# Optimization experiments

Measured on AMD Instinct MI355X. Metric: run time of the kernel, lower is better.

The kernel has to match this reference:

```python
import jax, jax.numpy as jnp
import numpy as np
import math

B, L, D_IN, D, H, NL, FF = 8, 1024, 32, 512, 8, 6, 64
DK = D // H

def _ln(x, g, b, eps=1e-5):
    m = jnp.mean(x, axis=-1, keepdims=True)
    v = jnp.mean((x - m) ** 2, axis=-1, keepdims=True)
    return (x - m) * jax.lax.rsqrt(v + eps) * g + b

def setup_inputs() -> dict:
    key = jax.random.key(0)
    ks = jax.random.split(key, 32)
    def nrm(k, shape, s=0.02):
        return jax.random.normal(k, shape, jnp.float32) * s
    x = jax.random.normal(ks[0], (B, L, D_IN), jnp.float32)
    mask = jnp.broadcast_to(jnp.tril(jnp.ones((L, L), jnp.int32))[None], (B, L, L))
    obs_time = jnp.arange(B * L, dtype=jnp.float32).reshape(B, L)
    inp = {
        "x": x, "mask": mask, "obs_time": obs_time,
        # embedding MLP: Linear(d_input,d) -> ReLU -> [Dropout] -> LayerNorm -> Linear(d,d)
        "emb_w1": nrm(ks[1], (D_IN, D)), "emb_b1": jnp.zeros((D,), jnp.float32),
        "emb_g": jnp.ones((D,), jnp.float32), "emb_beta": jnp.zeros((D,), jnp.float32),
        "emb_w2": nrm(ks[2], (D, D)), "emb_b2": jnp.zeros((D,), jnp.float32),
        # per-layer stacked params [NL, ...]
        "wq": nrm(ks[3], (NL, D, D)), "wk": nrm(ks[4], (NL, D, D)), "wv": nrm(ks[5], (NL, D, D)),
        "wo": nrm(ks[6], (NL, D, D)), "bo": jnp.zeros((NL, D), jnp.float32),
        "fw1": nrm(ks[7], (NL, D, FF)), "fb1": jnp.zeros((NL, FF), jnp.float32),
        "fw2": nrm(ks[8], (NL, FF, D)), "fb2": jnp.zeros((NL, D), jnp.float32),
        "g1": jnp.ones((NL, D), jnp.float32), "b1": jnp.zeros((NL, D), jnp.float32),
        "g2": jnp.ones((NL, D), jnp.float32), "b2": jnp.zeros((NL, D), jnp.float32),
    }
    return inp

def reference(x, mask, obs_time, emb_w1, emb_b1, emb_g, emb_beta, emb_w2, emb_b2,
              wq, wk, wv, wo, bo, fw1, fb1, fw2, fb2, g1, b1, g2, b2):
    # positional encoding: pe[...,0::2]=sin(t*div), pe[...,1::2]=cos(t*div)
    t = obs_time[..., None]  # [B,L,1]
    div = jnp.exp(jnp.arange(0, D, 2, dtype=jnp.float32) * (-math.log(10000.0) / D))
    pe = jnp.stack([jnp.sin(t * div), jnp.cos(t * div)], axis=-1).reshape(x.shape[0], x.shape[1], D)

    # embedding MLP (dropout = identity at eval)
    h = jax.nn.relu(x @ emb_w1 + emb_b1)
    h = _ln(h, emb_g, emb_beta)
    h = h @ emb_w2 + emb_b2
    h = h + pe

    Bx, Lx = h.shape[0], h.shape[1]
    scale = 1.0 / np.sqrt(DK).astype(np.float32)
    mask4 = (mask == 0)[:, None]  # [B,1,L,L]
    for i in range(NL):
        # self-attention
        q = (h @ wq[i]).reshape(Bx, Lx, H, DK).transpose(0, 2, 1, 3)  # bhld
        k = (h @ wk[i]).reshape(Bx, Lx, H, DK).transpose(0, 2, 1, 3)
        v = (h @ wv[i]).reshape(Bx, Lx, H, DK).transpose(0, 2, 1, 3)
        scores = jnp.einsum('bhqd,bhkd->bhqk', q, k) * scale
        scores = jnp.where(mask4, -jnp.inf, scores)
        attn = jax.nn.softmax(scores, axis=-1)
        o = jnp.einsum('bhqk,bhkd->bhqd', attn, v).transpose(0, 2, 1, 3).reshape(Bx, Lx, D)
        o = o @ wo[i] + bo[i]
        h = _ln(h + o, g1[i], b1[i])
        # feed-forward d -> 64 -> d
        f = jax.nn.relu(h @ fw1[i] + fb1[i]) @ fw2[i] + fb2[i]
        h = _ln(h + f, g2[i], b2[i])
    return h
```

## Files before the change

kernel.cpp:

```cpp
#include <hip/hip_runtime.h>
#include <math.h>

typedef unsigned short u16;
typedef unsigned int   u32;
typedef __bf16 bf16_t;
typedef bf16_t bf16x8 __attribute__((ext_vector_type(8)));
typedef float  f32x4  __attribute__((ext_vector_type(4)));
typedef u16    u16x8  __attribute__((ext_vector_type(8)));
typedef u16    u16x4  __attribute__((ext_vector_type(4)));

#define B_   8
#define L_   1024
#define DIN_ 32
#define D_   512
#define H_   8
#define NL_  6
#define FF_  64
#define M_   (B_*L_)
#define DD_  (D_*D_)

#define PE_COEF (-0.017988946039015984f)
#define SC2     (0.18033688011112042f)

__device__ __forceinline__ u16 f2bf(float f) {
  u32 u = __builtin_bit_cast(u32, f);
  u32 r = (u + 0x7FFFu + ((u >> 16) & 1u)) >> 16;
  return (u16)r;
}
__device__ __forceinline__ u16 f2bf_fast(float f) {
  u32 u = __builtin_bit_cast(u32, f);
  return (u16)((u + 0x8000u) >> 16);
}
__device__ __forceinline__ float bf2f(u16 v) {
  u32 u = ((u32)v) << 16;
  return __builtin_bit_cast(float, u);
}

#define GLOAD_LDS16(gp, lp) \
  __builtin_amdgcn_global_load_lds((const __attribute__((address_space(1))) u32*)(gp), \
                                   (__attribute__((address_space(3))) u32*)(lp), 16, 0, 0)

__global__ __launch_bounds__(256) void transpose_all(const float* __restrict__ wq, const float* __restrict__ wk,
                                                     const float* __restrict__ wv, const float* __restrict__ wo,
                                                     const float* __restrict__ ew2,
                                                     u16* __restrict__ qkvt, u16* __restrict__ wot,
                                                     u16* __restrict__ ew2t) {
  __shared__ float tile[32][33];
  int z = blockIdx.z;
  const float* src;
  u16* dst;
  if (z < 18) {
    int grp = z / 6, i = z % 6;
    src = (grp == 0 ? wq : grp == 1 ? wk : wv) + (size_t)i*DD_;
    dst = qkvt + (size_t)i*3*DD_ + (size_t)grp*DD_;
  } else if (z < 24) {
    int i = z - 18;
    src = wo + (size_t)i*DD_;
    dst = wot + (size_t)i*DD_;
  } else {
    src = ew2; dst = ew2t;
  }
  int k0 = blockIdx.y * 32, n0 = blockIdx.x * 32;
  int tx = threadIdx.x & 31, ty = threadIdx.x >> 5;
  #pragma unroll
  for (int i = 0; i < 4; ++i)
    tile[ty + i*8][tx] = src[(size_t)(k0 + ty + i*8)*512 + n0 + tx];
  __syncthreads();
  #pragma unroll
  for (int i = 0; i < 4; ++i)
    dst[(size_t)(n0 + ty + i*8)*512 + k0 + tx] = f2bf(tile[tx][ty + i*8]);
}

__global__ __launch_bounds__(256) void transpose_k(const float* __restrict__ W, u16* __restrict__ Wt,
                                                   int K, int N, size_t in_zs, size_t out_zs) {
  __shared__ float tile[32][33];
  size_t mi = (size_t)blockIdx.z * in_zs;
  size_t mo = (size_t)blockIdx.z * out_zs;
  int k0 = blockIdx.y * 32, n0 = blockIdx.x * 32;
  int tx = threadIdx.x & 31, ty = threadIdx.x >> 5;
  #pragma unroll
  for (int i = 0; i < 4; ++i)
    tile[ty + i*8][tx] = W[mi + (size_t)(k0 + ty + i*8)*N + n0 + tx];
  __syncthreads();
  #pragma unroll
  for (int i = 0; i < 4; ++i)
    Wt[mo + (size_t)(n0 + ty + i*8)*K + k0 + tx] = f2bf(tile[tx][ty + i*8]);
}

__global__ __launch_bounds__(256) void emb1_ln_kernel(const float* __restrict__ x, const float* __restrict__ W1,
                               const float* __restrict__ b1, const float* __restrict__ g,
                               const float* __restrict__ beta, u16* __restrict__ outb) {
  __shared__ float xs[DIN_];
  __shared__ float red[4];
  int m = blockIdx.x;
  int tid = threadIdx.x;
  if (tid < DIN_) xs[tid] = x[m*DIN_ + tid];
  __syncthreads();
  float v[2];
  #pragma unroll
  for (int r = 0; r < 2; ++r) {
    int n = tid + r*256;
    float acc = b1[n];
    #pragma unroll
    for (int k = 0; k < DIN_; ++k) acc += xs[k] * W1[k*D_ + n];
    v[r] = fmaxf(acc, 0.f);
  }
  float s = v[0] + v[1];
  #pragma unroll
  for (int off = 32; off > 0; off >>= 1) s += __shfl_down(s, off, 64);
  int wid = tid >> 6;
  if ((tid & 63) == 0) red[wid] = s;
  __syncthreads();
  float mean = (red[0] + red[1] + red[2] + red[3]) * (1.f/D_);
  float d0 = v[0] - mean, d1 = v[1] - mean;
  float vv = d0*d0 + d1*d1;
  #pragma unroll
  for (int off = 32; off > 0; off >>= 1) vv += __shfl_down(vv, off, 64);
  __syncthreads();
  if ((tid & 63) == 0) red[wid] = vv;
  __syncthreads();
  float var = (red[0] + red[1] + red[2] + red[3]) * (1.f/D_);
  float rstd = rsqrtf(var + 1e-5f);
  outb[(size_t)m*D_ + tid]       = f2bf(d0*rstd*g[tid]       + beta[tid]);
  outb[(size_t)m*D_ + tid + 256] = f2bf(d1*rstd*g[tid + 256] + beta[tid + 256]);
}

__global__ __launch_bounds__(256) void add_ln_kernel(const float* __restrict__ hin, const u16* __restrict__ res,
                              const float* __restrict__ g, const float* __restrict__ b,
                              float* __restrict__ outf, u16* __restrict__ outb) {
  int w = threadIdx.x >> 6, lane = threadIdx.x & 63;
  int m = blockIdx.x * 4 + w;
  const float* hr = hin + (size_t)m*D_;
  const u16*   rr = res + (size_t)m*D_;
  float v[8];
  float s = 0.f;
  #pragma unroll
  for (int i = 0; i < 8; ++i) {
    int c = lane + i*64;
    v[i] = hr[c] + bf2f(rr[c]);
    s += v[i];
  }
  #pragma unroll
  for (int off = 32; off > 0; off >>= 1) s += __shfl_xor(s, off, 64);
  float mean = s * (1.f/D_);
  float vs = 0.f;
  #pragma unroll
  for (int i = 0; i < 8; ++i) { v[i] -= mean; vs += v[i]*v[i]; }
  #pragma unroll
  for (int off = 32; off > 0; off >>= 1) vs += __shfl_xor(vs, off, 64);
  float rstd = rsqrtf(vs * (1.f/D_) + 1e-5f);
  #pragma unroll
  for (int i = 0; i < 8; ++i) {
    int c = lane + i*64;
    float o = v[i]*rstd*g[c] + b[c];
    outf[(size_t)m*D_ + c] = o;
    outb[(size_t)m*D_ + c] = f2bf(o);
  }
}

template<int BM, int BN, int EPI, bool WF, bool WB>
__global__ __launch_bounds__(256) void mgemm(const u16* __restrict__ A, const u16* __restrict__ Bt,
                            const float* __restrict__ bias, const float* __restrict__ extra,
                            float* __restrict__ Cf, u16* __restrict__ Cb,
                            int M, int N, int K) {
  constexpr int NBUF = 3;
  constexpr int LPT = BM/64 + BN/64;
  __shared__ __align__(16) u16 As[NBUF][BM*32];
  __shared__ __align__(16) u16 Bs[NBUF][BN*32];
  const int WR = BM/2, WC = BN/2, MR = WR/16, NR = WC/16;
  int nx = gridDim.x;
  int nwg = nx * gridDim.y;
  int flat = blockIdx.y * nx + blockIdx.x;
  int wid = (flat & 7) * (nwg >> 3) + (flat >> 3);
  int bm = (wid / nx) * BM, bn = (wid % nx) * BN;
  int tid = threadIdx.x, w = tid >> 6, l = tid & 63;
  int wr = w >> 1, wc = w & 1;
  int lq = l & 15, lg = l >> 4;
  f32x4 acc[MR][NR];
  #pragma unroll
  for (int m = 0; m < MR; ++m)
    #pragma unroll
    for (int n = 0; n < NR; ++n) acc[m][n] = f32x4{0.f,0.f,0.f,0.f};

  int srow = w*16 + (l >> 2);
  int scol = (l & 3)*8;

  auto stage = [&](int t, int bi) {
    int k0 = t << 5;
    #pragma unroll
    for (int i = 0; i < BM/64; ++i)
      GLOAD_LDS16(A + (size_t)(bm + i*64 + srow)*K + k0 + scol, &As[bi][i*2048 + w*512]);
    #pragma unroll
    for (int i = 0; i < BN/64; ++i)
      GLOAD_LDS16(Bt + (size_t)(bn + i*64 + srow)*K + k0 + scol, &Bs[bi][i*2048 + w*512]);
  };

  int nk = K >> 5;
  stage(0, 0);
  if (nk > 1) stage(1, 1);
  int bi = 0;
  #pragma unroll 1
  for (int t = 0; t < nk; ++t) {
    if (t + 1 < nk) {
      if constexpr (LPT == 2)      asm volatile("s_waitcnt vmcnt(2)" ::: "memory");
      else if constexpr (LPT == 3) asm volatile("s_waitcnt vmcnt(3)" ::: "memory");
      else if constexpr (LPT == 4) asm volatile("s_waitcnt vmcnt(4)" ::: "memory");
      else                         asm volatile("s_waitcnt vmcnt(0)" ::: "memory");
    } else {
      asm volatile("s_waitcnt vmcnt(0)" ::: "memory");
    }
    __builtin_amdgcn_s_barrier();
    __builtin_amdgcn_sched_barrier(0);
    if (t + 2 < nk) {
      int b2 = bi + 2; if (b2 >= NBUF) b2 -= NBUF;
      stage(t + 2, b2);
    }
    bf16x8 af[MR], bfr[NR];
    #pragma unroll
    for (int m = 0; m < MR; ++m)
      af[m] = *(const bf16x8*)&As[bi][(wr*WR + m*16 + lq)*32 + lg*8];
    #pragma unroll
    for (int n = 0; n < NR; ++n)
      bfr[n] = *(const bf16x8*)&Bs[bi][(wc*WC + n*16 + lq)*32 + lg*8];
    #pragma unroll
    for (int m = 0; m < MR; ++m)
      #pragma unroll
      for (int n = 0; n < NR; ++n)
        acc[m][n] = __builtin_amdgcn_mfma_f32_16x16x32_bf16(af[m], bfr[n], acc[m][n], 0, 0, 0);
    bi = (bi + 1 == NBUF) ? 0 : bi + 1;
  }

  #pragma unroll
  for (int m = 0; m < MR; ++m) {
    #pragma unroll
    for (int n = 0; n < NR; ++n) {
      #pragma unroll
      for (int r = 0; r < 4; ++r) {
        int row = bm + wr*WR + m*16 + lg*4 + r;
        int col = bn + wc*WC + n*16 + lq;
        float v = acc[m][n][r];
        if (EPI & 1) v += bias[col];
        if (EPI & 2) v = fmaxf(v, 0.f);
        if (EPI & 4) {
          float fr  = __expf((float)(col & ~1) * PE_COEF);
          float arg = extra[row] * fr;
          v += (col & 1) ? cosf(arg) : sinf(arg);
        }
        if (WF) Cf[(size_t)row*N + col] = v;
        if (WB) Cb[(size_t)row*N + col] = f2bf(v);
      }
    }
  }
}

__global__ __launch_bounds__(512) void ff_fused(const u16* __restrict__ Ain,
        const u16* __restrict__ fw1t, const float* __restrict__ fb1,
        const u16* __restrict__ fw2t, const float* __restrict__ fb2,
        const float* __restrict__ hres, const float* __restrict__ g,
        const float* __restrict__ bet, float* __restrict__ outf, u16* __restrict__ outb) {
  __shared__ __align__(16) u16 Asw[32*512];
  __shared__ __align__(16) u16 fls[32*72];
  __shared__ float part[32][4];
  int tid = threadIdx.x, w = tid >> 6, l = tid & 63;
  int lq = l & 15, lg = l >> 4;
  int bm = blockIdx.x * 32;
  #pragma unroll
  for (int i = 0; i < 4; ++i) {
    int lam = tid + i*512;
    int row = lam >> 6;
    int slot = lam & 63;
    int sslot = slot ^ (row & 7);
    GLOAD_LDS16(Ain + (size_t)(bm + row)*512 + sslot*8, Asw + lam*8);
  }
  asm volatile("s_waitcnt vmcnt(0)" ::: "memory");
  __syncthreads();
  {
    int mt = w >> 2, nt = w & 3;
    f32x4 facc = f32x4{0.f,0.f,0.f,0.f};
    const u16* bp = fw1t + (size_t)(nt*16 + lq)*512;
    int arow = mt*16 + lq;
    #pragma unroll
    for (int ks = 0; ks < 16; ++ks) {
      int slot = (ks*4 + lg) ^ (arow & 7);
      bf16x8 a = *(const bf16x8*)&Asw[arow*512 + slot*8];
      bf16x8 b = *(const bf16x8*)&bp[ks*32 + lg*8];
      facc = __builtin_amdgcn_mfma_f32_16x16x32_bf16(a, b, facc, 0, 0, 0);
    }
    float bias = fb1[nt*16 + lq];
    #pragma unroll
    for (int r = 0; r < 4; ++r)
      fls[(mt*16 + lg*4 + r)*72 + nt*16 + lq] = f2bf(fmaxf(facc[r] + bias, 0.f));
  }
  __syncthreads();
  int m0 = (w >> 2) * 16;
  int n0 = (w & 3) * 128;
  f32x4 acc[8];
  #pragma unroll
  for (int n = 0; n < 8; ++n) acc[n] = f32x4{0.f,0.f,0.f,0.f};
  #pragma unroll
  for (int ks = 0; ks < 2; ++ks) {
    bf16x8 a = *(const bf16x8*)&fls[(m0 + lq)*72 + ks*32 + lg*8];
    #pragma unroll
    for (int n = 0; n < 8; ++n) {
      bf16x8 b = *(const bf16x8*)&fw2t[(size_t)(n0 + n*16 + lq)*64 + ks*32 + lg*8];
      acc[n] = __builtin_amdgcn_mfma_f32_16x16x32_bf16(a, b, acc[n], 0, 0, 0);
    }
  }
  float v[8][4];
  float psum[4] = {0.f,0.f,0.f,0.f};
  #pragma unroll
  for (int n = 0; n < 8; ++n) {
    int col = n0 + n*16 + lq;
    float bias = fb2[col];
    #pragma unroll
    for (int r = 0; r < 4; ++r) {
      int row = bm + m0 + lg*4 + r;
      float t = acc[n][r] + bias + hres[(size_t)row*512 + col];
      v[n][r] = t;
      psum[r] += t;
    }
  }
  #pragma unroll
  for (int off = 1; off <= 8; off <<= 1)
    #pragma unroll
    for (int r = 0; r < 4; ++r) psum[r] += __shfl_xor(psum[r], off);
  if (lq == 0)
    #pragma unroll
    for (int r = 0; r < 4; ++r) part[m0 + lg*4 + r][w & 3] = psum[r];
  __syncthreads();
  float mean[4];
  #pragma unroll
  for (int r = 0; r < 4; ++r) {
    int row = m0 + lg*4 + r;
    mean[r] = (part[row][0] + part[row][1] + part[row][2] + part[row][3]) * (1.f/512.f);
  }
  __syncthreads();
  float pv[4] = {0.f,0.f,0.f,0.f};
  #pragma unroll
  for (int n = 0; n < 8; ++n)
    #pragma unroll
    for (int r = 0; r < 4; ++r) { v[n][r] -= mean[r]; pv[r] += v[n][r]*v[n][r]; }
  #pragma unroll
  for (int off = 1; off <= 8; off <<= 1)
    #pragma unroll
    for (int r = 0; r < 4; ++r) pv[r] += __shfl_xor(pv[r], off);
  if (lq == 0)
    #pragma unroll
    for (int r = 0; r < 4; ++r) part[m0 + lg*4 + r][w & 3] = pv[r];
  __syncthreads();
  #pragma unroll
  for (int r = 0; r < 4; ++r) {
    int lrow = m0 + lg*4 + r;
    float var = (part[lrow][0] + part[lrow][1] + part[lrow][2] + part[lrow][3]) * (1.f/512.f);
    float rstd = rsqrtf(var + 1e-5f);
    int row = bm + lrow;
    #pragma unroll
    for (int n = 0; n < 8; ++n) {
      int col = n0 + n*16 + lq;
      float o = v[n][r]*rstd*g[col] + bet[col];
      outf[(size_t)row*512 + col] = o;
      outb[(size_t)row*512 + col] = f2bf(o);
    }
  }
}

#define QS_ 1536
__global__ __launch_bounds__(256) void attn_kernel(const u16* __restrict__ Q, const u16* __restrict__ Kp,
                                                   const u16* __restrict__ V, u16* __restrict__ O) {
  __shared__ __align__(16) u16 Ks[2][64*72];
  __shared__ __align__(16) u16 Vt[2][64*72];
  __shared__ __align__(16) u16 Ps[4][16*72];
  int flat = blockIdx.y * 8 + blockIdx.x;
  int wid  = (flat & 7) * 64 + (flat >> 3);
  int pair = wid & 7, bh = wid >> 3;
  int b = bh >> 3, hh = bh & 7;
  int rowbase = b * L_, col0 = hh * 64;
  int tid = threadIdx.x, w = tid >> 6, l = tid & 63;
  int lq = l & 15, lg = l >> 4;

  int krow = tid >> 3, kseg = tid & 7;
  int vg = tid >> 5, vd2 = (tid & 31) * 2;

  u16x8 kr0, kr1;
  u32 vr[8];
  u16x8 oc16;
  #pragma unroll
  for (int i = 0; i < 8; ++i) oc16[i] = 0x3F80u;
  const bf16x8 onesA = __builtin_bit_cast(bf16x8, oc16);

  #define LOADKV(t) { \
    kr0 = *(const u16x8*)&Kp[(size_t)(rowbase + (t)*64 + krow)*QS_ + col0 + kseg*8]; \
    kr1 = *(const u16x8*)&Kp[(size_t)(rowbase + (t)*64 + krow + 32)*QS_ + col0 + kseg*8]; \
    _Pragma("unroll") \
    for (int i_ = 0; i_ < 8; ++i_) \
      vr[i_] = *(const u32*)&V[(size_t)(rowbase + (t)*64 + vg*8 + i_)*QS_ + col0 + vd2]; }

  #define WRITE_LDS(bb) { \
    *(u16x8*)&Ks[bb][krow*72 + kseg*8]        = kr0; \
    *(u16x8*)&Ks[bb][(krow + 32)*72 + kseg*8] = kr1; \
    u16x8 vlo, vhi; \
    _Pragma("unroll") \
    for (int i_ = 0; i_ < 8; ++i_) { vlo[i_] = (u16)(vr[i_] & 0xffffu); vhi[i_] = (u16)(vr[i_] >> 16); } \
    *(u16x8*)&Vt[bb][vd2*72 + vg*8]     = vlo; \
    *(u16x8*)&Vt[bb][(vd2+1)*72 + vg*8] = vhi; }

  LOADKV(0);

  #pragma unroll 1
  for (int half = 0; half < 2; ++half) {
    int qt = half ? (15 - pair) : pair;
    int qrow = rowbase + qt*64 + w*16 + lq;
    bf16x8 qa0 = *(const bf16x8*)&Q[(size_t)qrow*QS_ + col0 + lg*8];
    bf16x8 qa1 = *(const bf16x8*)&Q[(size_t)qrow*QS_ + col0 + 32 + lg*8];
    float m_s[4];
    f32x4 o[4], o4;
    #pragma unroll
    for (int r = 0; r < 4; ++r) m_s[r] = -1e30f;
    #pragma unroll
    for (int n = 0; n < 4; ++n) o[n] = f32x4{0.f,0.f,0.f,0.f};
    o4 = f32x4{0.f,0.f,0.f,0.f};

    __syncthreads();
    WRITE_LDS(0);

    #pragma unroll 1
    for (int kt = 0; kt <= qt; ++kt) {
      int buf = kt & 1;
      __syncthreads();
      int nt = (kt < qt) ? (kt + 1) : (half == 0 ? 0 : -1);
      if (nt >= 0) LOADKV(nt);

      f32x4 t4[4];
      __builtin_amdgcn_s_setprio(1);
      #pragma unroll
      for (int f = 0; f < 4; ++f) {
        bf16x8 k0 = *(const bf16x8*)&Ks[buf][(f*16 + lq)*72 + lg*8];
        bf16x8 k1 = *(const bf16x8*)&Ks[buf][(f*16 + lq)*72 + 32 + lg*8];
        f32x4 z = f32x4{0.f,0.f,0.f,0.f};
        z = __builtin_amdgcn_mfma_f32_16x16x32_bf16(qa0, k0, z, 0, 0, 0);
        z = __builtin_amdgcn_mfma_f32_16x16x32_bf16(qa1, k1, z, 0, 0, 0);
        #pragma unroll
        for (int r = 0; r < 4; ++r) t4[f][r] = z[r] * SC2;
      }
      __builtin_amdgcn_s_setprio(0);
      if (kt == qt) {
        #pragma unroll
        for (int f = 0; f < 4; ++f) {
          int kvg = f*16 + lq;
          #pragma unroll
          for (int r = 0; r < 4; ++r)
            if (kvg > w*16 + lg*4 + r) t4[f][r] = -1e30f;
        }
      }
      float tm[4];
      bool need = false;
      #pragma unroll
      for (int r = 0; r < 4; ++r) {
        float vv = fmaxf(fmaxf(t4[0][r], t4[1][r]), fmaxf(t4[2][r], t4[3][r]));
        vv = fmaxf(vv, __shfl_xor(vv, 1));
        vv = fmaxf(vv, __shfl_xor(vv, 2));
        vv = fmaxf(vv, __shfl_xor(vv, 4));
        vv = fmaxf(vv, __shfl_xor(vv, 8));
        tm[r] = vv;
        need = need || (vv > m_s[r]);
      }
      if (__any(need)) {
        float corr[4];
        #pragma unroll
        for (int r = 0; r < 4; ++r) {
          float mn = fmaxf(m_s[r], tm[r]);
          corr[r] = __builtin_amdgcn_exp2f(m_s[r] - mn);
          m_s[r] = mn;
        }
        int bsrc = (lq >> 2)*16 + lq;
        float c0 = __shfl(corr[0], bsrc);
        float c1 = __shfl(corr[1], bsrc);
        float c2 = __shfl(corr[2], bsrc);
        float c3 = __shfl(corr[3], bsrc);
        float cb = (lq & 2) ? ((lq & 1) ? c3 : c2) : ((lq & 1) ? c1 : c0);
        #pragma unroll
        for (int n = 0; n < 4; ++n)
          #pragma unroll
          for (int r = 0; r < 4; ++r) o[n][r] *= cb;
        #pragma unroll
        for (int r = 0; r < 4; ++r) o4[r] *= cb;
      }
      #pragma unroll
      for (int r = 0; r < 4; ++r) {
        int prow = (lg*4 + r)*72;
        Ps[w][prow + lq]      = f2bf_fast(__builtin_amdgcn_exp2f(t4[0][r] - m_s[r]));
        Ps[w][prow + 16 + lq] = f2bf_fast(__builtin_amdgcn_exp2f(t4[1][r] - m_s[r]));
        Ps[w][prow + 32 + lq] = f2bf_fast(__builtin_amdgcn_exp2f(t4[2][r] - m_s[r]));
        Ps[w][prow + 48 + lq] = f2bf_fast(__builtin_amdgcn_exp2f(t4[3][r] - m_s[r]));
      }
      bf16x8 pB0 = *(const bf16x8*)&Ps[w][lq*72 + lg*8];
      bf16x8 pB1 = *(const bf16x8*)&Ps[w][lq*72 + 32 + lg*8];
      __builtin_amdgcn_s_setprio(1);
      o4 = __builtin_amdgcn_mfma_f32_16x16x32_bf16(onesA, pB0, o4, 0, 0, 0);
      o4 = __builtin_amdgcn_mfma_f32_16x16x32_bf16(onesA, pB1, o4, 0, 0, 0);
      #pragma unroll
      for (int n = 0; n < 4; ++n) {
        bf16x8 vA0 = *(const bf16x8*)&Vt[buf][(n*16 + lq)*72 + lg*8];
        bf16x8 vA1 = *(const bf16x8*)&Vt[buf][(n*16 + lq)*72 + 32 + lg*8];
        o[n] = __builtin_amdgcn_mfma_f32_16x16x32_bf16(vA0, pB0, o[n], 0, 0, 0);
        o[n] = __builtin_amdgcn_mfma_f32_16x16x32_bf16(vA1, pB1, o[n], 0, 0, 0);
      }
      __builtin_amdgcn_s_setprio(0);
      if (kt < qt) WRITE_LDS(buf ^ 1);
    }
    float inv = 1.f / o4[0];
    #pragma unroll
    for (int n = 0; n < 4; ++n) {
      u16x4 pk;
      #pragma unroll
      for (int r = 0; r < 4; ++r) pk[r] = f2bf(o[n][r] * inv);
      *(u16x4*)&O[(size_t)(rowbase + qt*64 + w*16 + lq)*D_ + col0 + n*16 + lg*4] = pk;
    }
  }
  #undef LOADKV
  #undef WRITE_LDS
}

extern "C" void kernel_launch(void* const* d_in, const int* in_sizes, int n_in,
                              void* d_out, int out_size, void* d_ws, size_t ws_size,
                              hipStream_t stream) {
  (void)in_sizes; (void)n_in; (void)out_size; (void)ws_size;
  const float* x      = (const float*)d_in[0];
  const float* obs    = (const float*)d_in[2];
  const float* emb_w1 = (const float*)d_in[3];
  const float* emb_b1 = (const float*)d_in[4];
  const float* emb_g  = (const float*)d_in[5];
  const float* emb_be = (const float*)d_in[6];
  const float* emb_w2 = (const float*)d_in[7];
  const float* emb_b2 = (const float*)d_in[8];
  const float* wq  = (const float*)d_in[9];
  const float* wk  = (const float*)d_in[10];
  const float* wv  = (const float*)d_in[11];
  const float* wo  = (const float*)d_in[12];
  const float* bo  = (const float*)d_in[13];
  const float* fw1 = (const float*)d_in[14];
  const float* fb1 = (const float*)d_in[15];
  const float* fw2 = (const float*)d_in[16];
  const float* fb2 = (const float*)d_in[17];
  const float* g1  = (const float*)d_in[18];
  const float* b1  = (const float*)d_in[19];
  const float* g2  = (const float*)d_in[20];
  const float* b2  = (const float*)d_in[21];
  float* out = (float*)d_out;

  float* hf  = (float*)d_ws;
  u16* hb    = (u16*)(hf + (size_t)M_*D_);
  u16* qkvb  = hb + (size_t)M_*D_;
  u16* ob    = qkvb + (size_t)M_*3*D_;
  u16* ofb   = ob + (size_t)M_*D_;
  u16* qkvt  = ofb + (size_t)M_*D_;
  u16* wot   = qkvt + (size_t)18*DD_;
  u16* ew2t  = wot + (size_t)6*DD_;
  u16* fw1t  = ew2t + (size_t)DD_;
  u16* fw2t  = fw1t + (size_t)6*D_*FF_;

  transpose_all<<<dim3(16,16,25), 256, 0, stream>>>(wq, wk, wv, wo, emb_w2, qkvt, wot, ew2t);
  transpose_k<<<dim3(2,16,6),  256, 0, stream>>>(fw1, fw1t, 512,  64, (size_t)D_*FF_, (size_t)D_*FF_);
  transpose_k<<<dim3(16,2,6),  256, 0, stream>>>(fw2, fw2t,  64, 512, (size_t)D_*FF_, (size_t)D_*FF_);

  emb1_ln_kernel<<<M_, 256, 0, stream>>>(x, emb_w1, emb_b1, emb_g, emb_be, ob);
  mgemm<128,128,5,true,true><<<dim3(4,64), 256, 0, stream>>>(ob, ew2t, emb_b2, obs, hf, hb, M_, D_, D_);

  for (int i = 0; i < NL_; ++i) {
    mgemm<128,128,0,false,true><<<dim3(12,64), 256, 0, stream>>>(hb, qkvt + (size_t)i*3*DD_,
        nullptr, nullptr, nullptr, qkvb, M_, 3*D_, D_);
    attn_kernel<<<dim3(8, B_*H_), 256, 0, stream>>>(qkvb, qkvb + D_, qkvb + 2*D_, ob);
    mgemm<128,128,1,false,true><<<dim3(4,64), 256, 0, stream>>>(ob, wot + (size_t)i*DD_,
        bo + i*D_, nullptr, nullptr, ofb, M_, D_, D_);
    add_ln_kernel<<<M_/4, 256, 0, stream>>>(hf, ofb, g1 + i*D_, b1 + i*D_, hf, hb);
    ff_fused<<<M_/32, 512, 0, stream>>>(hb, fw1t + (size_t)i*D_*FF_, fb1 + i*FF_,
        fw2t + (size_t)i*D_*FF_, fb2 + i*D_, hf, g2 + i*D_, b2 + i*D_,
        (i == NL_-1) ? out : hf, hb);
  }
}
```

Baseline: 799.6 us.

## Replace tiled GEMM with row-block GEMM and fuse out-projection with add+LayerNorm

Replaces the 128x128 LDS-pipelined GEMM with a row-block GEMM: each block loads a 32x512 A tile into swizzled LDS once, and each wave streams its B columns straight from global memory into registers with double buffering. The out-projection GEMM now adds the residual and applies LayerNorm in its epilogue, which removes the separate add_ln kernel and the bf16 intermediate buffer. The aim is to cut a kernel launch and one round trip of the activation tensor per layer. The cost is that B is re-read from global or L2 by every row block with no LDS reuse, and only 256 to 768 blocks run with heavy register use.

```diff
diff --git a/kernel.cpp b/kernel.cpp
--- a/kernel.cpp
+++ b/kernel.cpp
@@ -125,131 +125,159 @@
   outb[(size_t)m*D_ + tid + 256] = f2bf(d1*rstd*g[tid + 256] + beta[tid + 256]);
 }
 
-__global__ __launch_bounds__(256) void add_ln_kernel(const float* __restrict__ hin, const u16* __restrict__ res,
-                              const float* __restrict__ g, const float* __restrict__ b,
-                              float* __restrict__ outf, u16* __restrict__ outb) {
-  int w = threadIdx.x >> 6, lane = threadIdx.x & 63;
-  int m = blockIdx.x * 4 + w;
-  const float* hr = hin + (size_t)m*D_;
-  const u16*   rr = res + (size_t)m*D_;
-  float v[8];
-  float s = 0.f;
+template<int EPI, bool LNF, bool WF, bool WB>
+__global__ __launch_bounds__(256) void rowgemm(const u16* __restrict__ A, const u16* __restrict__ Bt,
+        const float* __restrict__ bias, const float* __restrict__ extra,
+        const float* __restrict__ hres, const float* __restrict__ g, const float* __restrict__ bet,
+        float* __restrict__ Cf, u16* __restrict__ Cb, int N) {
+  constexpr int K = 512;
+  __shared__ __align__(16) u16 Asw[32*512];
+  __shared__ float part[32][4];
+  int tid = threadIdx.x, w = tid >> 6, l = tid & 63;
+  int lq = l & 15, lg = l >> 4;
+  int bx = blockIdx.x;
+  int mb = (bx & 7) * 32 + (bx >> 3);
+  int bm = mb * 32;
+  int nb = blockIdx.y * 512 + w * 128;
+
   #pragma unroll
   for (int i = 0; i < 8; ++i) {
-    int c = lane + i*64;
-    v[i] = hr[c] + bf2f(rr[c]);
-    s += v[i];
-  }
-  #pragma unroll
-  for (int off = 32; off > 0; off >>= 1) s += __shfl_xor(s, off, 64);
-  float mean = s * (1.f/D_);
-  float vs = 0.f;
-  #pragma unroll
-  for (int i = 0; i < 8; ++i) { v[i] -= mean; vs += v[i]*v[i]; }
-  #pragma unroll
-  for (int off = 32; off > 0; off >>= 1) vs += __shfl_xor(vs, off, 64);
-  float rstd = rsqrtf(vs * (1.f/D_) + 1e-5f);
-  #pragma unroll
-  for (int i = 0; i < 8; ++i) {
-    int c = lane + i*64;
-    float o = v[i]*rstd*g[c] + b[c];
-    outf[(size_t)m*D_ + c] = o;
-    outb[(size_t)m*D_ + c] = f2bf(o);
-  }
-}
-
-template<int BM, int BN, int EPI, bool WF, bool WB>
-__global__ __launch_bounds__(256) void mgemm(const u16* __restrict__ A, const u16* __restrict__ Bt,
-                            const float* __restrict__ bias, const float* __restrict__ extra,
-                            float* __restrict__ Cf, u16* __restrict__ Cb,
-                            int M, int N, int K) {
-  constexpr int NBUF = 3;
-  constexpr int LPT = BM/64 + BN/64;
-  __shared__ __align__(16) u16 As[NBUF][BM*32];
-  __shared__ __align__(16) u16 Bs[NBUF][BN*32];
-  const int WR = BM/2, WC = BN/2, MR = WR/16, NR = WC/16;
-  int nx = gridDim.x;
-  int nwg = nx * gridDim.y;
-  int flat = blockIdx.y * nx + blockIdx.x;
-  int wid = (flat & 7) * (nwg >> 3) + (flat >> 3);
-  int bm = (wid / nx) * BM, bn = (wid % nx) * BN;
-  int tid = threadIdx.x, w = tid >> 6, l = tid & 63;
-  int wr = w >> 1, wc = w & 1;
-  int lq = l & 15, lg = l >> 4;
-  f32x4 acc[MR][NR];
-  #pragma unroll
-  for (int m = 0; m < MR; ++m)
-    #pragma unroll
-    for (int n = 0; n < NR; ++n) acc[m][n] = f32x4{0.f,0.f,0.f,0.f};
-
-  int srow = w*16 + (l >> 2);
-  int scol = (l & 3)*8;
-
-  auto stage = [&](int t, int bi) {
-    int k0 = t << 5;
-    #pragma unroll
-    for (int i = 0; i < BM/64; ++i)
-      GLOAD_LDS16(A + (size_t)(bm + i*64 + srow)*K + k0 + scol, &As[bi][i*2048 + w*512]);
-    #pragma unroll
-    for (int i = 0; i < BN/64; ++i)
-      GLOAD_LDS16(Bt + (size_t)(bn + i*64 + srow)*K + k0 + scol, &Bs[bi][i*2048 + w*512]);
-  };
-
-  int nk = K >> 5;
-  stage(0, 0);
-  if (nk > 1) stage(1, 1);
-  int bi = 0;
-  #pragma unroll 1
-  for (int t = 0; t < nk; ++t) {
-    if (t + 1 < nk) {
-      if constexpr (LPT == 2)      asm volatile("s_waitcnt vmcnt(2)" ::: "memory");
-      else if constexpr (LPT == 3) asm volatile("s_waitcnt vmcnt(3)" ::: "memory");
-      else if constexpr (LPT == 4) asm volatile("s_waitcnt vmcnt(4)" ::: "memory");
-      else                         asm volatile("s_waitcnt vmcnt(0)" ::: "memory");
-    } else {
-      asm volatile("s_waitcnt vmcnt(0)" ::: "memory");
-    }
-    __builtin_amdgcn_s_barrier();
-    __builtin_amdgcn_sched_barrier(0);
-    if (t + 2 < nk) {
-      int b2 = bi + 2; if (b2 >= NBUF) b2 -= NBUF;
-      stage(t + 2, b2);
-    }
-    bf16x8 af[MR], bfr[NR];
-    #pragma unroll
-    for (int m = 0; m < MR; ++m)
-      af[m] = *(const bf16x8*)&As[bi][(wr*WR + m*16 + lq)*32 + lg*8];
-    #pragma unroll
-    for (int n = 0; n < NR; ++n)
-      bfr[n] = *(const bf16x8*)&Bs[bi][(wc*WC + n*16 + lq)*32 + lg*8];
-    #pragma unroll
-    for (int m = 0; m < MR; ++m)
-      #pragma unroll
-      for (int n = 0; n < NR; ++n)
-        acc[m][n] = __builtin_amdgcn_mfma_f32_16x16x32_bf16(af[m], bfr[n], acc[m][n], 0, 0, 0);
-    bi = (bi + 1 == NBUF) ? 0 : bi + 1;
-  }
-
-  #pragma unroll
-  for (int m = 0; m < MR; ++m) {
-    #pragma unroll
-    for (int n = 0; n < NR; ++n) {
+    int lam = tid + i*256;
+    int row = lam >> 6, slot = lam & 63;
+    GLOAD_LDS16(A + (size_t)(bm + row)*K + (slot ^ (row & 7))*8, Asw + lam*8);
+  }
+  asm volatile("s_waitcnt vmcnt(0)" ::: "memory");
+  __syncthreads();
+
+  const u16* bbase = Bt + (size_t)(nb + lq)*K + lg*8;
+  u16x8 bb[2][8];
+  #pragma unroll
+  for (int n = 0; n < 8; ++n) bb[0][n] = *(const u16x8*)(bbase + n*16*K);
+  f32x4 acc[2][8];
+  #pragma unroll
+  for (int m = 0; m < 2; ++m)
+    #pragma unroll
+    for (int n = 0; n < 8; ++n) acc[m][n] = f32x4{0.f,0.f,0.f,0.f};
+
+  #pragma unroll 2
+  for (int t = 0; t < 16; ++t) {
+    int cur = t & 1;
+    if (t < 15) {
+      int k1 = (t + 1) * 32;
+      #pragma unroll
+      for (int n = 0; n < 8; ++n)
+        bb[cur ^ 1][n] = *(const u16x8*)(bbase + n*16*K + k1);
+    }
+    int ks = (t*4 + lg) ^ (lq & 7);
+    bf16x8 a0 = *(const bf16x8*)&Asw[lq*512 + ks*8];
+    bf16x8 a1 = *(const bf16x8*)&Asw[(16 + lq)*512 + ks*8];
+    #pragma unroll
+    for (int n = 0; n < 8; ++n) {
+      bf16x8 bn = __builtin_bit_cast(bf16x8, bb[cur][n]);
+      acc[0][n] = __builtin_amdgcn_mfma_f32_16x16x32_bf16(a0, bn, acc[0][n], 0, 0, 0);
+      acc[1][n] = __builtin_amdgcn_mfma_f32_16x16x32_bf16(a1, bn, acc[1][n], 0, 0, 0);
+    }
+  }
+
+  #pragma unroll
+  for (int m = 0; m < 2; ++m) {
+    #pragma unroll
+    for (int n = 0; n < 8; ++n) {
       #pragma unroll
       for (int r = 0; r < 4; ++r) {
-        int row = bm + wr*WR + m*16 + lg*4 + r;
-        int col = bn + wc*WC + n*16 + lq;
+        int row = bm + m*16 + lg*4 + r;
+        int col = nb + n*16 + lq;
         float v = acc[m][n][r];
         if (EPI & 1) v += bias[col];
-        if (EPI & 2) v = fmaxf(v, 0.f);
         if (EPI & 4) {
           float fr  = __expf((float)(col & ~1) * PE_COEF);
           float arg = extra[row] * fr;
           v += (col & 1) ? cosf(arg) : sinf(arg);
         }
-        if (WF) Cf[(size_t)row*N + col] = v;
-        if (WB) Cb[(size_t)row*N + col] = f2bf(v);
-      }
-    }
+        if (LNF) v += hres[(size_t)row*512 + col];
+        acc[m][n][r] = v;
+      }
+    }
+  }
+  if (LNF) {
+    float ps[2][4] = {{0.f,0.f,0.f,0.f},{0.f,0.f,0.f,0.f}};
+    #pragma unroll
+    for (int m = 0; m < 2; ++m)
+      #pragma unroll
+      for (int n = 0; n < 8; ++n)
+        #pragma unroll
+        for (int r = 0; r < 4; ++r) ps[m][r] += acc[m][n][r];
+    #pragma unroll
+    for (int off = 1; off <= 8; off <<= 1)
+      #pragma unroll
+      for (int m = 0; m < 2; ++m)
+        #pragma unroll
+        for (int r = 0; r < 4; ++r) ps[m][r] += __shfl_xor(ps[m][r], off);
+    if (lq == 0)
+      #pragma unroll
+      for (int m = 0; m < 2; ++m)
+        #pragma unroll
+        for (int r = 0; r < 4; ++r) part[m*16 + lg*4 + r][w] = ps[m][r];
+    __syncthreads();
+    float mean[2][4];
+    #pragma unroll
+    for (int m = 0; m < 2; ++m)
+      #pragma unroll
+      for (int r = 0; r < 4; ++r) {
+        int rw = m*16 + lg*4 + r;
+        mean[m][r] = (part[rw][0] + part[rw][1] + part[rw][2] + part[rw][3]) * (1.f/512.f);
+      }
+    __syncthreads();
+    float pv[2][4] = {{0.f,0.f,0.f,0.f},{0.f,0.f,0.f,0.f}};
+    #pragma unroll
+    for (int m = 0; m < 2; ++m)
+      #pragma unroll
+      for (int n = 0; n < 8; ++n)
+        #pragma unroll
+        for (int r = 0; r < 4; ++r) {
+          acc[m][n][r] -= mean[m][r];
+          pv[m][r] += acc[m][n][r]*acc[m][n][r];
+        }
+    #pragma unroll
+    for (int off = 1; off <= 8; off <<= 1)
+      #pragma unroll
+      for (int m = 0; m < 2; ++m)
+        #pragma unroll
+        for (int r = 0; r < 4; ++r) pv[m][r] += __shfl_xor(pv[m][r], off);
+    if (lq == 0)
+      #pragma unroll
+      for (int m = 0; m < 2; ++m)
+        #pragma unroll
+        for (int r = 0; r < 4; ++r) part[m*16 + lg*4 + r][w] = pv[m][r];
+    __syncthreads();
+    #pragma unroll
+    for (int m = 0; m < 2; ++m)
+      #pragma unroll
+      for (int r = 0; r < 4; ++r) {
+        int rw = m*16 + lg*4 + r;
+        float var = (part[rw][0] + part[rw][1] + part[rw][2] + part[rw][3]) * (1.f/512.f);
+        float rstd = rsqrtf(var + 1e-5f);
+        int row = bm + rw;
+        #pragma unroll
+        for (int n = 0; n < 8; ++n) {
+          int col = nb + n*16 + lq;
+          float o = acc[m][n][r]*rstd*g[col] + bet[col];
+          if (WF) Cf[(size_t)row*512 + col] = o;
+          if (WB) Cb[(size_t)row*512 + col] = f2bf(o);
+        }
+      }
+  } else {
+    #pragma unroll
+    for (int m = 0; m < 2; ++m)
+      #pragma unroll
+      for (int n = 0; n < 8; ++n)
+        #pragma unroll
+        for (int r = 0; r < 4; ++r) {
+          int row = bm + m*16 + lg*4 + r;
+          int col = nb + n*16 + lq;
+          if (WF) Cf[(size_t)row*N + col] = acc[m][n][r];
+          if (WB) Cb[(size_t)row*N + col] = f2bf(acc[m][n][r]);
+        }
   }
 }
 
@@ -552,8 +580,7 @@
   u16* hb    = (u16*)(hf + (size_t)M_*D_);
   u16* qkvb  = hb + (size_t)M_*D_;
   u16* ob    = qkvb + (size_t)M_*3*D_;
-  u16* ofb   = ob + (size_t)M_*D_;
-  u16* qkvt  = ofb + (size_t)M_*D_;
+  u16* qkvt  = ob + (size_t)M_*D_;
   u16* wot   = qkvt + (size_t)18*DD_;
   u16* ew2t  = wot + (size_t)6*DD_;
   u16* fw1t  = ew2t + (size_t)DD_;
@@ -564,15 +591,15 @@
   transpose_k<<<dim3(16,2,6),  256, 0, stream>>>(fw2, fw2t,  64, 512, (size_t)D_*FF_, (size_t)D_*FF_);
 
   emb1_ln_kernel<<<M_, 256, 0, stream>>>(x, emb_w1, emb_b1, emb_g, emb_be, ob);
-  mgemm<128,128,5,true,true><<<dim3(4,64), 256, 0, stream>>>(ob, ew2t, emb_b2, obs, hf, hb, M_, D_, D_);
+  rowgemm<5,false,true,true><<<dim3(256,1), 256, 0, stream>>>(ob, ew2t, emb_b2, obs,
+      nullptr, nullptr, nullptr, hf, hb, 512);
 
   for (int i = 0; i < NL_; ++i) {
-    mgemm<128,128,0,false,true><<<dim3(12,64), 256, 0, stream>>>(hb, qkvt + (size_t)i*3*DD_,
-        nullptr, nullptr, nullptr, qkvb, M_, 3*D_, D_);
+    rowgemm<0,false,false,true><<<dim3(256,3), 256, 0, stream>>>(hb, qkvt + (size_t)i*3*DD_,
+        nullptr, nullptr, nullptr, nullptr, nullptr, nullptr, qkvb, 1536);
     attn_kernel<<<dim3(8, B_*H_), 256, 0, stream>>>(qkvb, qkvb + D_, qkvb + 2*D_, ob);
-    mgemm<128,128,1,false,true><<<dim3(4,64), 256, 0, stream>>>(ob, wot + (size_t)i*DD_,
-        bo + i*D_, nullptr, nullptr, ofb, M_, D_, D_);
-    add_ln_kernel<<<M_/4, 256, 0, stream>>>(hf, ofb, g1 + i*D_, b1 + i*D_, hf, hb);
+    rowgemm<1,true,true,true><<<dim3(256,1), 256, 0, stream>>>(ob, wot + (size_t)i*DD_,
+        bo + i*D_, nullptr, hf, g1 + i*D_, b1 + i*D_, hf, hb, 512);
     ff_fused<<<M_/32, 512, 0, stream>>>(hb, fw1t + (size_t)i*D_*FF_, fb1 + i*FF_,
         fw2t + (size_t)i*D_*FF_, fb2 + i*D_, hf, g2 + i*D_, b2 + i*D_,
         (i == NL_-1) ? out : hf, hb);
```

Result: slower. 998.4 us (+24.9%).
